# Performance work log

Measured on AMD Instinct MI355X. Metric: run time of the kernel, lower is better.

Reference implementation:

```python
import jax, jax.numpy as jnp
import numpy as np

EPS = 1e-5

def rms_norm(x):
    # SimpleRMSNorm (no learned weight), as used inside BitLinear158
    return x * jax.lax.rsqrt(jnp.mean(x * x, axis=-1, keepdims=True) + EPS)

def act_quant(x):
    # int8 absmax quantization per last-dim row, with straight-through estimator
    scale = 127.0 / jnp.clip(jnp.max(jnp.abs(x), axis=-1, keepdims=True), 1e-5)
    q = jnp.clip(jnp.round(x * scale), -128.0, 127.0) / scale
    return x + jax.lax.stop_gradient(q - x)

def weight_quant(w):
    # ternary {-1,0,1} absmean quantization, with straight-through estimator
    scale = 1.0 / jnp.clip(jnp.mean(jnp.abs(w)), 1e-5)
    q = jnp.clip(jnp.round(w * scale), -1.0, 1.0) / scale
    return w + jax.lax.stop_gradient(q - w)

def bitlinear158(x, w, b):
    xq = act_quant(rms_norm(x))          # [b,s,d_in]
    wq = weight_quant(w)                 # [d_out,d_in]
    return jnp.einsum('bsd,od->bso', xq, wq) + b

def layer_norm(x, g, b):
    mu = jnp.mean(x, axis=-1, keepdims=True)
    var = jnp.mean((x - mu) ** 2, axis=-1, keepdims=True)
    return (x - mu) * jax.lax.rsqrt(var + EPS) * g + b

def setup_inputs() -> dict:
    key = jax.random.key(0)
    ks = jax.random.split(key, 3)
    d, inner = 2048, 8192
    x = jax.random.normal(ks[0], (4, 2048, d), dtype=jnp.float32)
    w1 = jax.random.normal(ks[1], (inner, d), dtype=jnp.float32) * 0.02
    b1 = jnp.zeros((inner,), jnp.float32)
    ln_g = jnp.ones((inner,), jnp.float32)
    ln_b = jnp.zeros((inner,), jnp.float32)
    w2 = jax.random.normal(ks[2], (d, inner), dtype=jnp.float32) * 0.02
    b2 = jnp.zeros((d,), jnp.float32)
    return {"x": x, "w1": w1, "b1": b1, "ln_g": ln_g, "ln_b": ln_b, "w2": w2, "b2": b2}

def reference(x, w1, b1, ln_g, ln_b, w2, b2):
    h = jax.nn.silu(bitlinear158(x, w1, b1))        # project_in: BitLinear158 + SiLU
    h = jax.nn.gelu(h, approximate=False)            # nn.GELU (exact erf form)
    h = layer_norm(h, ln_g, ln_b)                    # nn.LayerNorm(inner_dim)
    return bitlinear158(h, w2, b2)                   # BitLinear158 out projection
```

## Files before the change

kernel.cpp:

```cpp
#include <hip/hip_runtime.h>
#include <hip/hip_bf16.h>
#include <math.h>

typedef __bf16 bf16_t;
typedef __bf16 bf16x4 __attribute__((ext_vector_type(4)));
typedef int i32x4 __attribute__((ext_vector_type(4)));

#define AS1 __attribute__((address_space(1)))
#define AS3 __attribute__((address_space(3)))

__device__ __forceinline__ void gl_lds16(const char* g, char* l) {
  __builtin_amdgcn_global_load_lds((const AS1 void*)g, (AS3 void*)l, 16, 0, 0);
}

__device__ __forceinline__ unsigned pack4i(float a, float b, float c, float d) {
  return ((unsigned)(unsigned char)(int)a) | ((unsigned)(unsigned char)(int)b << 8) |
         ((unsigned)(unsigned char)(int)c << 16) | ((unsigned)(unsigned char)(int)d << 24);
}

__device__ __forceinline__ float block_sum_f(float v) {
  __shared__ float sb[4];
  #pragma unroll
  for (int o = 32; o; o >>= 1) v += __shfl_xor(v, o);
  if ((threadIdx.x & 63) == 0) sb[threadIdx.x >> 6] = v;
  __syncthreads();
  v = sb[0] + sb[1] + sb[2] + sb[3];
  __syncthreads();
  return v;
}
__device__ __forceinline__ float block_max_f(float v) {
  __shared__ float sm[4];
  #pragma unroll
  for (int o = 32; o; o >>= 1) v = fmaxf(v, __shfl_xor(v, o));
  if ((threadIdx.x & 63) == 0) sm[threadIdx.x >> 6] = v;
  __syncthreads();
  v = fmaxf(fmaxf(sm[0], sm[1]), fmaxf(sm[2], sm[3]));
  __syncthreads();
  return v;
}

__global__ __launch_bounds__(256) void wabs_partial(const float* __restrict__ w, int n4,
                                                    double* __restrict__ part) {
  const float4* w4 = (const float4*)w;
  double s = 0.0;
  const int stride = gridDim.x * blockDim.x;
  for (int i = blockIdx.x * blockDim.x + threadIdx.x; i < n4; i += stride) {
    float4 v = w4[i];
    s += (double)fabsf(v.x) + (double)fabsf(v.y) + (double)fabsf(v.z) + (double)fabsf(v.w);
  }
  #pragma unroll
  for (int o = 32; o; o >>= 1) s += __shfl_xor(s, o);
  __shared__ double sd[4];
  if ((threadIdx.x & 63) == 0) sd[threadIdx.x >> 6] = s;
  __syncthreads();
  if (threadIdx.x == 0) part[blockIdx.x] = sd[0] + sd[1] + sd[2] + sd[3];
}

__global__ __launch_bounds__(256) void wabs_final(const double* __restrict__ part, int np,
                                                  double n, float* __restrict__ fwout) {
  double s = 0.0;
  for (int i = threadIdx.x; i < np; i += blockDim.x) s += part[i];
  #pragma unroll
  for (int o = 32; o; o >>= 1) s += __shfl_xor(s, o);
  __shared__ double sd[4];
  if ((threadIdx.x & 63) == 0) sd[threadIdx.x >> 6] = s;
  __syncthreads();
  if (threadIdx.x == 0) {
    double mean = (sd[0] + sd[1] + sd[2] + sd[3]) / n;
    fwout[0] = (float)fmax(mean, 1e-5);
  }
}

__global__ __launch_bounds__(256) void quant_w(const float* __restrict__ w,
                                               const float* __restrict__ fw,
                                               char* __restrict__ wq, int n4) {
  int i = blockIdx.x * blockDim.x + threadIdx.x;
  if (i >= n4) return;
  const float s = 1.0f / fw[0];
  float4 v = ((const float4*)w)[i];
  ((unsigned*)wq)[i] = pack4i(fminf(fmaxf(rintf(v.x * s), -1.f), 1.f),
                              fminf(fmaxf(rintf(v.y * s), -1.f), 1.f),
                              fminf(fmaxf(rintf(v.z * s), -1.f), 1.f),
                              fminf(fmaxf(rintf(v.w * s), -1.f), 1.f));
}

__global__ __launch_bounds__(256) void rms_quant_x(const float* __restrict__ x,
                                                   char* __restrict__ xq,
                                                   float* __restrict__ fx, int K) {
  const int row = blockIdx.x, t = threadIdx.x;
  const size_t base = (size_t)row * K;
  float v[8];
  float ss = 0.f;
  #pragma unroll
  for (int j = 0; j < 2; j++) {
    float4 lv = *(const float4*)(x + base + j * 1024 + t * 4);
    v[j*4+0] = lv.x; v[j*4+1] = lv.y; v[j*4+2] = lv.z; v[j*4+3] = lv.w;
  }
  #pragma unroll
  for (int i = 0; i < 8; i++) ss += v[i] * v[i];
  ss = block_sum_f(ss);
  const float r = 1.0f / sqrtf(ss / (float)K + 1e-5f);
  float amax = 0.f;
  #pragma unroll
  for (int i = 0; i < 8; i++) { v[i] *= r; amax = fmaxf(amax, fabsf(v[i])); }
  amax = block_max_f(amax);
  amax = fmaxf(amax, 1e-5f);
  const float scale = 127.0f / amax;
  #pragma unroll
  for (int j = 0; j < 2; j++) {
    float q[4];
    #pragma unroll
    for (int e = 0; e < 4; e++)
      q[e] = fminf(fmaxf(rintf(v[j*4+e] * scale), -128.f), 127.f);
    *(unsigned*)(xq + base + j * 1024 + t * 4) = pack4i(q[0], q[1], q[2], q[3]);
  }
  if (t == 0) fx[row] = amax / 127.0f;
}

__global__ __launch_bounds__(256) void ln_rms_quant(const bf16_t* __restrict__ h,
                                                    char* __restrict__ hq,
                                                    const float* __restrict__ g,
                                                    const float* __restrict__ bb,
                                                    float* __restrict__ fh, int N) {
  const int row = blockIdx.x, t = threadIdx.x;
  const size_t base = (size_t)row * N;
  float v[32];
  float s = 0.f, ss = 0.f;
  #pragma unroll
  for (int j = 0; j < 8; j++) {
    const int col = j * 1024 + t * 4;
    bf16x4 q = *(const bf16x4*)(h + base + col);
    v[j*4+0] = (float)q[0]; v[j*4+1] = (float)q[1];
    v[j*4+2] = (float)q[2]; v[j*4+3] = (float)q[3];
  }
  #pragma unroll
  for (int i = 0; i < 32; i++) { s += v[i]; ss += v[i] * v[i]; }
  s = block_sum_f(s);
  ss = block_sum_f(ss);
  const float mu = s / (float)N;
  const float var = ss / (float)N - mu * mu;
  const float rstd = 1.0f / sqrtf(var + 1e-5f);
  float ss2 = 0.f;
  #pragma unroll
  for (int j = 0; j < 8; j++) {
    const int col = j * 1024 + t * 4;
    float4 gv = *(const float4*)(g + col);
    float4 bv = *(const float4*)(bb + col);
    float y0 = (v[j*4+0] - mu) * rstd * gv.x + bv.x;
    float y1 = (v[j*4+1] - mu) * rstd * gv.y + bv.y;
    float y2 = (v[j*4+2] - mu) * rstd * gv.z + bv.z;
    float y3 = (v[j*4+3] - mu) * rstd * gv.w + bv.w;
    v[j*4+0] = y0; v[j*4+1] = y1; v[j*4+2] = y2; v[j*4+3] = y3;
    ss2 += y0*y0 + y1*y1 + y2*y2 + y3*y3;
  }
  ss2 = block_sum_f(ss2);
  const float r2 = 1.0f / sqrtf(ss2 / (float)N + 1e-5f);
  float amax = 0.f;
  #pragma unroll
  for (int i = 0; i < 32; i++) { v[i] *= r2; amax = fmaxf(amax, fabsf(v[i])); }
  amax = block_max_f(amax);
  amax = fmaxf(amax, 1e-5f);
  const float scale = 127.0f / amax;
  #pragma unroll
  for (int j = 0; j < 8; j++) {
    const int col = j * 1024 + t * 4;
    float q[4];
    #pragma unroll
    for (int e = 0; e < 4; e++)
      q[e] = fminf(fmaxf(rintf(v[j*4+e] * scale), -128.f), 127.f);
    *(unsigned*)(hq + base + col) = pack4i(q[0], q[1], q[2], q[3]);
  }
  if (t == 0) fh[row] = amax / 127.0f;
}

template<int EPI, bool STORE_BF16>
__global__ __launch_bounds__(256, 2) void gemm256(const char* __restrict__ A,
                                                  const char* __restrict__ B,
                                                  const float* __restrict__ rowf,
                                                  const float* __restrict__ wf,
                                                  const float* __restrict__ bias,
                                                  float* __restrict__ Cf,
                                                  bf16_t* __restrict__ Cb,
                                                  int M, int N, int K) {
  __shared__ char smem[73728];

  const int ntile = N >> 7;
  const int cpx = gridDim.x >> 3;
  const int bid = blockIdx.x;
  const int xcd = bid & 7, local = bid >> 3;
  int wg;
  const int mrows = cpx / ntile;
  if (mrows * ntile == cpx && mrows > 0) {
    const int bm_l = local % mrows, bn_i = local / mrows;
    wg = (xcd * mrows + bm_l) * ntile + bn_i;
  } else {
    wg = xcd * cpx + local;
  }
  const int bm = wg / ntile, bn = wg % ntile;
  const int tm = bm << 8, tn = bn << 7;

  const int tid = threadIdx.x;
  const int w = tid >> 6, lane = tid & 63;
  const int wm = w >> 1, wn = w & 1;
  const int ln15 = lane & 15;

  const int srow = lane >> 2;
  const int scol = (((lane & 3) ^ ((lane >> 3) & 3)) << 4);
  const size_t KS = (size_t)K;
  const char* pAst = A + (size_t)(tm + w * 16 + srow) * KS + scol;
  const char* pBst = B + (size_t)(tn + w * 16 + srow) * KS + scol;
  const size_t r64 = (size_t)64 * KS;
  const int dW = w * 1024;

  const int foff = ln15 * 64 + ((((lane >> 4) ^ ((ln15 >> 1) & 3))) << 4);

  i32x4 acc[8][4] = {};
  const int NT = K >> 6;

#define SB __builtin_amdgcn_sched_barrier(0)
#define BAR { SB; __builtin_amdgcn_s_barrier(); SB; }
#define VM(n) asm volatile("s_waitcnt vmcnt(" #n ")" ::: "memory")
#define ST(bb, kt) { const size_t ko = (size_t)(kt) * 64;                    \
    char* ab = smem + (bb) * 24576 + dW;                                     \
    char* bbp = smem + (bb) * 24576 + 16384 + dW;                            \
    gl_lds16(pAst + ko,            ab);                                      \
    gl_lds16(pAst + r64 + ko,      ab + 4096);                               \
    gl_lds16(pAst + 2 * r64 + ko,  ab + 8192);                               \
    gl_lds16(pAst + 3 * r64 + ko,  ab + 12288);                              \
    gl_lds16(pBst + ko,            bbp);                                     \
    gl_lds16(pBst + r64 + ko,      bbp + 4096); }

  ST(0, 0); ST(1, 1);

  int cur = 0;
  for (int t = 0; t < NT; ++t) {
    if (t + 1 < NT) { VM(6); } else { VM(0); }
    BAR;
    int s2 = cur + 2; if (s2 >= 3) s2 -= 3;
    if (t + 2 < NT) ST(s2, t + 2);
    const char* sA = smem + cur * 24576;
    const char* sBp = sA + 16384;
    i32x4 afr[8], bfr[4];
    #pragma unroll
    for (int m4 = 0; m4 < 8; m4++)
      afr[m4] = *(const i32x4*)(sA + (wm * 8 + m4) * 1024 + foff);
    #pragma unroll
    for (int n2 = 0; n2 < 4; n2++)
      bfr[n2] = *(const i32x4*)(sBp + (wn * 4 + n2) * 1024 + foff);
    __builtin_amdgcn_s_setprio(1);
    #pragma unroll
    for (int m4 = 0; m4 < 8; m4++)
      #pragma unroll
      for (int n2 = 0; n2 < 4; n2++)
        acc[m4][n2] = __builtin_amdgcn_mfma_i32_16x16x64_i8(afr[m4], bfr[n2],
                                                            acc[m4][n2], 0, 0, 0);
    __builtin_amdgcn_s_setprio(0);
    cur = cur + 1 == 3 ? 0 : cur + 1;
  }
#undef ST
#undef VM

  const float fwv = wf[0];
  const int rq = (lane >> 4) << 2;
  float rsc[8][4];
  #pragma unroll
  for (int m = 0; m < 8; m++)
    #pragma unroll
    for (int r = 0; r < 4; r++)
      rsc[m][r] = rowf[tm + wm * 128 + m * 16 + rq + r] * fwv;

  #pragma unroll
  for (int m = 0; m < 8; m++) {
    #pragma unroll
    for (int n = 0; n < 4; n++) {
      const int col = tn + wn * 64 + n * 16 + ln15;
      const float bv = bias[col];
      #pragma unroll
      for (int r = 0; r < 4; r++) {
        const int row = tm + wm * 128 + m * 16 + rq + r;
        float val = (float)acc[m][n][r] * rsc[m][r] + bv;
        if (EPI == 1) {
          float sl = val / (1.0f + __expf(-val));
          val = 0.5f * sl * (1.0f + erff(sl * 0.70710678118654752f));
        }
        if (STORE_BF16) Cb[(size_t)row * N + col] = (bf16_t)val;
        else            Cf[(size_t)row * N + col] = val;
      }
    }
  }
}

extern "C" void kernel_launch(void* const* d_in, const int* in_sizes, int n_in,
                              void* d_out, int out_size, void* d_ws, size_t ws_size,
                              hipStream_t stream) {
  const float* x   = (const float*)d_in[0];
  const float* w1  = (const float*)d_in[1];
  const float* b1  = (const float*)d_in[2];
  const float* lng = (const float*)d_in[3];
  const float* lnb = (const float*)d_in[4];
  const float* w2  = (const float*)d_in[5];
  const float* b2  = (const float*)d_in[6];
  float* out = (float*)d_out;

  const int inner = in_sizes[2];
  const int d     = in_sizes[1] / inner;
  const int M     = in_sizes[0] / d;

  char* ws = (char*)d_ws;
  size_t off = 0;
  double* part = (double*)(ws + off); off += 1024 * 8;
  float*  fw   = (float*)(ws + off);  off += 256;
  float*  fx   = (float*)(ws + off);  off += (size_t)M * 4;
  float*  fh   = (float*)(ws + off);  off += (size_t)M * 4;
  char*   w1q  = ws + off;            off += (size_t)inner * d;
  char*   w2q  = ws + off;            off += (size_t)inner * d;

  int MC = M;
  while (MC > 256 && off + (size_t)MC * ((size_t)d + 3 * (size_t)inner) > ws_size) MC >>= 1;
  char*   xq = ws + off;              off += (size_t)MC * d;
  bf16_t* h  = (bf16_t*)(ws + off);   off += (size_t)MC * inner * 2;
  char*   hq = ws + off;

  const int nw = inner * d;
  const int n4 = nw / 4;

  wabs_partial<<<1024, 256, 0, stream>>>(w1, n4, part);
  wabs_final<<<1, 256, 0, stream>>>(part, 1024, (double)nw, fw + 0);
  wabs_partial<<<1024, 256, 0, stream>>>(w2, n4, part);
  wabs_final<<<1, 256, 0, stream>>>(part, 1024, (double)nw, fw + 1);
  quant_w<<<n4 / 256, 256, 0, stream>>>(w1, fw + 0, w1q, n4);
  quant_w<<<n4 / 256, 256, 0, stream>>>(w2, fw + 1, w2q, n4);

  for (int mc = 0; mc < M; mc += MC) {
    rms_quant_x<<<MC, 256, 0, stream>>>(x + (size_t)mc * d, xq, fx, d);

    const int g1 = (MC / 256) * (inner / 128);
    gemm256<1, true><<<g1, 256, 0, stream>>>(xq, w1q, fx, fw + 0, b1,
                                             nullptr, h, MC, inner, d);

    ln_rms_quant<<<MC, 256, 0, stream>>>(h, hq, lng, lnb, fh, inner);

    const int g2 = (MC / 256) * (d / 128);
    gemm256<0, false><<<g2, 256, 0, stream>>>(hq, w2q, fh, fw + 1, b2,
                                              out + (size_t)mc * d, nullptr, MC, d, inner);
  }
}
```

Baseline: 460.2 us.

## Give each wave private LDS buffers to drop block barriers in GEMM loop

Each wave now loads its own A (128 rows) and B (64 rows) slices into a private triple-buffered LDS region, so the main K loop needs only per-wave vmcnt waits and no workgroup barriers. This doubles LDS use to 144KB and cuts occupancy to one block per CU. A and B tiles that waves used to share are now loaded redundantly, which doubles global-to-LDS traffic. It also relies on the wave's own global_load_lds completing before its LDS reads, with no barrier between them.

```diff
diff --git a/kernel.cpp b/kernel.cpp
--- a/kernel.cpp
+++ b/kernel.cpp
@@ -174,7 +174,7 @@
 }
 
 template<int EPI, bool STORE_BF16>
-__global__ __launch_bounds__(256, 2) void gemm256(const char* __restrict__ A,
+__global__ __launch_bounds__(256, 1) void gemm256(const char* __restrict__ A,
                                                   const char* __restrict__ B,
                                                   const float* __restrict__ rowf,
                                                   const float* __restrict__ wf,
@@ -182,7 +182,7 @@
                                                   float* __restrict__ Cf,
                                                   bf16_t* __restrict__ Cb,
                                                   int M, int N, int K) {
-  __shared__ char smem[73728];
+  __shared__ char smem[147456];
 
   const int ntile = N >> 7;
   const int cpx = gridDim.x >> 3;
@@ -207,46 +207,40 @@
   const int srow = lane >> 2;
   const int scol = (((lane & 3) ^ ((lane >> 3) & 3)) << 4);
   const size_t KS = (size_t)K;
-  const char* pAst = A + (size_t)(tm + w * 16 + srow) * KS + scol;
-  const char* pBst = B + (size_t)(tn + w * 16 + srow) * KS + scol;
-  const size_t r64 = (size_t)64 * KS;
-  const int dW = w * 1024;
+  const char* pAst = A + (size_t)(tm + wm * 128 + srow) * KS + scol;
+  const char* pBst = B + (size_t)(tn + wn * 64 + srow) * KS + scol;
+  const size_t r16 = (size_t)16 * KS;
+  char* myb = smem + w * 36864;
 
   const int foff = ln15 * 64 + ((((lane >> 4) ^ ((ln15 >> 1) & 3))) << 4);
 
   i32x4 acc[8][4] = {};
   const int NT = K >> 6;
 
-#define SB __builtin_amdgcn_sched_barrier(0)
-#define BAR { SB; __builtin_amdgcn_s_barrier(); SB; }
 #define VM(n) asm volatile("s_waitcnt vmcnt(" #n ")" ::: "memory")
 #define ST(bb, kt) { const size_t ko = (size_t)(kt) * 64;                    \
-    char* ab = smem + (bb) * 24576 + dW;                                     \
-    char* bbp = smem + (bb) * 24576 + 16384 + dW;                            \
-    gl_lds16(pAst + ko,            ab);                                      \
-    gl_lds16(pAst + r64 + ko,      ab + 4096);                               \
-    gl_lds16(pAst + 2 * r64 + ko,  ab + 8192);                               \
-    gl_lds16(pAst + 3 * r64 + ko,  ab + 12288);                              \
-    gl_lds16(pBst + ko,            bbp);                                     \
-    gl_lds16(pBst + r64 + ko,      bbp + 4096); }
+    char* dst = myb + (bb) * 12288;                                          \
+    _Pragma("unroll") for (int m4 = 0; m4 < 8; m4++)                         \
+      gl_lds16(pAst + m4 * r16 + ko, dst + m4 * 1024);                       \
+    _Pragma("unroll") for (int n2 = 0; n2 < 4; n2++)                         \
+      gl_lds16(pBst + n2 * r16 + ko, dst + 8192 + n2 * 1024); }
 
   ST(0, 0); ST(1, 1);
 
   int cur = 0;
   for (int t = 0; t < NT; ++t) {
-    if (t + 1 < NT) { VM(6); } else { VM(0); }
-    BAR;
     int s2 = cur + 2; if (s2 >= 3) s2 -= 3;
-    if (t + 2 < NT) ST(s2, t + 2);
-    const char* sA = smem + cur * 24576;
-    const char* sBp = sA + 16384;
+    if (t + 2 < NT) { ST(s2, t + 2); VM(24); }
+    else if (t + 1 < NT) { VM(12); }
+    else { VM(0); }
+    const char* sA = myb + cur * 12288;
     i32x4 afr[8], bfr[4];
     #pragma unroll
     for (int m4 = 0; m4 < 8; m4++)
-      afr[m4] = *(const i32x4*)(sA + (wm * 8 + m4) * 1024 + foff);
+      afr[m4] = *(const i32x4*)(sA + m4 * 1024 + foff);
     #pragma unroll
     for (int n2 = 0; n2 < 4; n2++)
-      bfr[n2] = *(const i32x4*)(sBp + (wn * 4 + n2) * 1024 + foff);
+      bfr[n2] = *(const i32x4*)(sA + 8192 + n2 * 1024 + foff);
     __builtin_amdgcn_s_setprio(1);
     #pragma unroll
     for (int m4 = 0; m4 < 8; m4++)
```

New measurement: 627.9 us. 1.36x slower.
